# Kernel optimization log

Measured on AMD Instinct MI355X. Metric: run time of the kernel, lower is better.

## Reference

```python
import jax, jax.numpy as jnp
import numpy as np

N_NODES = 50000
N_EDGES = 800000
D = 128
LN_EPS = 1e-5


def setup_inputs() -> dict:
    key = jax.random.key(0)
    ks = jax.random.split(key, 8)
    s = 1.0 / np.sqrt(D)
    return {
        "x": jax.random.normal(ks[0], (N_NODES, D), jnp.float32),
        "edge_index": jax.random.randint(ks[1], (2, N_EDGES), 0, N_NODES, jnp.int64),
        "W1l": jax.random.normal(ks[2], (D, D), jnp.float32) * s,
        "b1l": jnp.zeros((D,), jnp.float32),
        "W1r": jax.random.normal(ks[3], (D, D), jnp.float32) * s,
        "W2l": jax.random.normal(ks[4], (D, D), jnp.float32) * s,
        "b2l": jnp.zeros((D,), jnp.float32),
        "W2r": jax.random.normal(ks[5], (D, D), jnp.float32) * s,
        "ln_w": jnp.ones((D,), jnp.float32),
        "ln_b": jnp.zeros((D,), jnp.float32),
    }


def _sage_conv(h, edge_index, Wl, bl, Wr):
    # PyG SAGEConv (mean aggr): out = lin_l(mean_{j in N(i)} h_j) + lin_r(h_i)
    src, dst = edge_index[0], edge_index[1]
    n = h.shape[0]
    msg_sum = jax.ops.segment_sum(h[src], dst, num_segments=n)      # [N, D]
    cnt = jax.ops.segment_sum(jnp.ones_like(src, h.dtype), dst, num_segments=n)
    mean = msg_sum / jnp.maximum(cnt, 1.0)[:, None]                  # 0 for isolated
    return mean @ Wl.T + bl + h @ Wr.T


def _layer_norm(h, w, b):
    mu = jnp.mean(h, axis=-1, keepdims=True)
    var = jnp.mean(jnp.square(h - mu), axis=-1, keepdims=True)
    return (h - mu) * jax.lax.rsqrt(var + LN_EPS) * w + b


def reference(x, edge_index, W1l, b1l, W1r, W2l, b2l, W2r, ln_w, ln_b):
    h = jax.nn.relu(_sage_conv(x, edge_index, W1l, b1l, W1r))
    h = jax.nn.relu(_sage_conv(h, edge_index, W2l, b2l, W2r))
    return _layer_norm(h, ln_w, ln_b)
```

## Files before the change

### kernel.cpp

```cpp
#include <hip/hip_runtime.h>

#define DN 128
#define LS 136

typedef short s16x8 __attribute__((ext_vector_type(8)));
typedef float f32x4 __attribute__((ext_vector_type(4)));

__device__ __forceinline__ float bf2f(unsigned short u) {
    union { unsigned int i; float f; } v; v.i = ((unsigned int)u) << 16; return v.f;
}
__device__ __forceinline__ unsigned short f2bf(float f) {
    union { float f; unsigned int i; } v; v.f = f;
    unsigned int r = v.i + 0x7fffu + ((v.i >> 16) & 1u);
    return (unsigned short)(r >> 16);
}
__device__ __forceinline__ float lo16(unsigned int u) { return bf2f((unsigned short)(u & 0xffffu)); }
__device__ __forceinline__ float hi16(unsigned int u) { return bf2f((unsigned short)(u >> 16)); }
__device__ __forceinline__ unsigned int pack2(float x, float y) {
    return (unsigned int)f2bf(x) | ((unsigned int)f2bf(y) << 16);
}
__device__ __forceinline__ float ldx(const void* p, size_t i, int f32) {
    return f32 ? ((const float*)p)[i] : bf2f(((const unsigned short*)p)[i]);
}

__global__ void k_diag(unsigned short* out, int cnt, float val) {
    unsigned short v = f2bf(val);
    for (int i = blockIdx.x * blockDim.x + threadIdx.x; i < cnt; i += gridDim.x * blockDim.x)
        out[i] = v;
}

__global__ void k_probe(const void* x, const void* w, const int* e, int* flags) {
    int g = blockIdx.x * 256 + threadIdx.x;
    const unsigned short* xu = (const unsigned short*)x;
    int hitx = 0, hitw = 0, hite = 0;
    for (int i = g; i < 65536; i += 32768)
        if ((xu[i] & 0x7F80u) == 0x7F80u) hitx = 1;
    const unsigned short* wu = (const unsigned short*)w;
    if (g < 16384 && (wu[g] & 0x7F80u) == 0x7F80u) hitw = 1;
    if (g < 1000 && e[2 * g + 1] != 0) hite = 1;
    if (hitx) atomicOr(&flags[0], 1);
    if (hitw) atomicOr(&flags[2], 1);
    if (hite) atomicOr(&flags[1], 1);
}


__global__ __launch_bounds__(1024) void k_packhist(
        const int* e, const void* x,
        const void* W1l, const void* W1r, const void* W2l, const void* W2r,
        const void* b1l, const void* b2l, const void* lnw, const void* lnb,
        const int* flags, unsigned int* packed, int* cnt,
        unsigned int* h1, unsigned int* wb, float* biasf, float* lnf,
        int E, int n, int cc) {
    __shared__ int hist[256];
    const int t = threadIdx.x, b = blockIdx.x;
    const int nthr = gridDim.x * 1024;
    const int g = b * 1024 + t;
    if (t < 256) hist[t] = 0;
    __syncthreads();
    const int is64 = (flags[1] == 0);
    const int xf = flags[0];
    const int wf = flags[2];
    const int b0 = b * 4096;
#pragma unroll
    for (int k = 0; k < 4; ++k) {
        int i = b0 + t + k * 1024;
        if (i < E) {
            int d = is64 ? e[2 * (E + i)] : e[E + i];
            int s = is64 ? e[2 * i] : e[i];
            if ((unsigned)s >= (unsigned)n) s = 0;
            unsigned int key = ((unsigned)d < (unsigned)n)
                             ? (((unsigned)d << 16) | (unsigned)s) : 0xFFFF0000u;
            packed[i] = key;
            atomicAdd(&hist[key >> 24], 1);
        }
    }
    if (xf) {
        const float* xp = (const float*)x;
        for (int i = g; i < cc; i += nthr) {
            float2 f = *(const float2*)(xp + 2 * (size_t)i);
            h1[i] = pack2(f.x, f.y);
        }
    } else {
        const unsigned int* xp = (const unsigned int*)x;
        for (int i = g; i < cc; i += nthr) h1[i] = xp[i];
    }
    for (int i = g; i < 32768; i += nthr) {
        int m = i >> 13, el = i & 8191;
        const void* W = (m == 0) ? W1l : (m == 1) ? W1r : (m == 2) ? W2l : W2r;
        unsigned int v;
        if (wf) {
            float2 f = *(const float2*)((const float*)W + 2 * (size_t)el);
            v = pack2(f.x, f.y);
        } else {
            v = ((const unsigned int*)W)[el];
        }
        wb[(size_t)m * 8192 + el] = v;
    }
    if (g < 512) {
        float v;
        if (g < 128)      v = ldx(b1l, g, wf);
        else if (g < 256) v = ldx(b2l, g - 128, wf);
        else if (g < 384) v = ldx(lnw, g - 256, wf);
        else              v = ldx(lnb, g - 384, wf);
        if (g < 256) biasf[g] = v; else lnf[g - 256] = v;
    }
    __syncthreads();
    if (t < 256 && hist[t]) atomicAdd(&cnt[t], hist[t]);
}

__device__ __forceinline__ void scan_cnt(const int* cnt, int* sbase, int t) {
    if (t < 64) {
        int c0 = cnt[4 * t], c1 = cnt[4 * t + 1], c2 = cnt[4 * t + 2], c3 = cnt[4 * t + 3];
        int tot = c0 + c1 + c2 + c3, pre = tot;
#pragma unroll
        for (int off = 1; off < 64; off <<= 1) {
            int u = __shfl_up(pre, off, 64);
            if (t >= off) pre += u;
        }
        int e0 = pre - tot;
        sbase[4 * t] = e0; sbase[4 * t + 1] = e0 + c0;
        sbase[4 * t + 2] = e0 + c0 + c1; sbase[4 * t + 3] = e0 + c0 + c1 + c2;
        if (t == 63) sbase[256] = pre;
    }
}

__global__ __launch_bounds__(1024) void k_p1scat(const unsigned int* in, const int* cnt,
                                                 int* rsv, unsigned int* out, int E) {
    __shared__ int hist[256], lcur[256], gbase[256], sbase[257];
    int t = threadIdx.x;
    int b0 = blockIdx.x * 4096;
    int nb = E - b0; if (nb > 4096) nb = 4096;
    if (t < 256) hist[t] = 0;
    __syncthreads();
    unsigned int v[4];
#pragma unroll
    for (int k = 0; k < 4; ++k) {
        int i = t + k * 1024;
        v[k] = (i < nb) ? in[b0 + i] : 0u;
        if (i < nb) atomicAdd(&hist[v[k] >> 24], 1);
    }
    scan_cnt(cnt, sbase, t);
    __syncthreads();
    if (t < 256) {
        lcur[t] = 0;
        if (hist[t]) gbase[t] = sbase[t] + atomicAdd(&rsv[t], hist[t]);
    }
    __syncthreads();
#pragma unroll
    for (int k = 0; k < 4; ++k) {
        int i = t + k * 1024;
        if (i < nb) {
            unsigned int d = v[k] >> 24;
            int p = atomicAdd(&lcur[d], 1);
            out[gbase[d] + p] = v[k];
        }
    }
}

__global__ __launch_bounds__(1024) void k_p2(const unsigned int* in, const int* cnt,
                                             int* rowp, int* col, int n) {
    __shared__ int hist[256], cur[256], sbase[257];
    int t = threadIdx.x;
    int b = blockIdx.x;
    if (t < 256) hist[t] = 0;
    scan_cnt(cnt, sbase, t);
    __syncthreads();
    int lo = sbase[b], hi = sbase[b + 1];
    if (b == 0 && t == 0) rowp[n] = sbase[196];
    for (int i = lo + t; i < hi; i += 1024)
        atomicAdd(&hist[(in[i] >> 16) & 0xFFu], 1);
    __syncthreads();
    if (t < 64) {
        int h0 = hist[4 * t], h1 = hist[4 * t + 1], h2 = hist[4 * t + 2], h3 = hist[4 * t + 3];
        int tot = h0 + h1 + h2 + h3;
        int pre = tot;
#pragma unroll
        for (int off = 1; off < 64; off <<= 1) {
            int u = __shfl_up(pre, off, 64);
            if (t >= off) pre += u;
        }
        int e0 = pre - tot;
        int e1 = e0 + h0, e2 = e1 + h1, e3 = e2 + h2;
        cur[4 * t] = e0; cur[4 * t + 1] = e1; cur[4 * t + 2] = e2; cur[4 * t + 3] = e3;
        int d0 = b * 256 + 4 * t;
        if (d0 < n)     rowp[d0]     = lo + e0;
        if (d0 + 1 < n) rowp[d0 + 1] = lo + e1;
        if (d0 + 2 < n) rowp[d0 + 2] = lo + e2;
        if (d0 + 3 < n) rowp[d0 + 3] = lo + e3;
    }
    __syncthreads();
    for (int i = lo + t; i < hi; i += 1024) {
        unsigned int v = in[i];
        int p = atomicAdd(&cur[(v >> 16) & 0xFFu], 1);
        col[lo + p] = (int)(v & 0xFFFFu);
    }
}

__global__ void k_gather(const int* rowp, const int* col, const unsigned int* hp,
                         unsigned int* M, int n) {
    int row = blockIdx.x * 4 + (threadIdx.x >> 6);
    if (row >= n) return;
    const int L = threadIdx.x & 63;
    int b = rowp[row], e = rowp[row + 1];
    float s0 = 0.f, s1 = 0.f;
    for (int base = b; base < e; base += 64) {
        int cnt = e - base; if (cnt > 64) cnt = 64;
        int myc = (L < cnt) ? col[base + L] : 0;
        int j = 0;
        for (; j + 8 <= cnt; j += 8) {
            int a0 = __shfl(myc, j + 0, 64);
            int a1 = __shfl(myc, j + 1, 64);
            int a2 = __shfl(myc, j + 2, 64);
            int a3 = __shfl(myc, j + 3, 64);
            int a4 = __shfl(myc, j + 4, 64);
            int a5 = __shfl(myc, j + 5, 64);
            int a6 = __shfl(myc, j + 6, 64);
            int a7 = __shfl(myc, j + 7, 64);
            unsigned int u0 = hp[(size_t)a0 * 64 + L];
            unsigned int u1 = hp[(size_t)a1 * 64 + L];
            unsigned int u2 = hp[(size_t)a2 * 64 + L];
            unsigned int u3 = hp[(size_t)a3 * 64 + L];
            unsigned int u4 = hp[(size_t)a4 * 64 + L];
            unsigned int u5 = hp[(size_t)a5 * 64 + L];
            unsigned int u6 = hp[(size_t)a6 * 64 + L];
            unsigned int u7 = hp[(size_t)a7 * 64 + L];
            s0 += lo16(u0); s1 += hi16(u0);
            s0 += lo16(u1); s1 += hi16(u1);
            s0 += lo16(u2); s1 += hi16(u2);
            s0 += lo16(u3); s1 += hi16(u3);
            s0 += lo16(u4); s1 += hi16(u4);
            s0 += lo16(u5); s1 += hi16(u5);
            s0 += lo16(u6); s1 += hi16(u6);
            s0 += lo16(u7); s1 += hi16(u7);
        }
        for (; j + 4 <= cnt; j += 4) {
            int a0 = __shfl(myc, j + 0, 64);
            int a1 = __shfl(myc, j + 1, 64);
            int a2 = __shfl(myc, j + 2, 64);
            int a3 = __shfl(myc, j + 3, 64);
            unsigned int u0 = hp[(size_t)a0 * 64 + L];
            unsigned int u1 = hp[(size_t)a1 * 64 + L];
            unsigned int u2 = hp[(size_t)a2 * 64 + L];
            unsigned int u3 = hp[(size_t)a3 * 64 + L];
            s0 += lo16(u0); s1 += hi16(u0);
            s0 += lo16(u1); s1 += hi16(u1);
            s0 += lo16(u2); s1 += hi16(u2);
            s0 += lo16(u3); s1 += hi16(u3);
        }
        for (; j < cnt; ++j) {
            int s = __shfl(myc, j, 64);
            unsigned int u = hp[(size_t)s * 64 + L];
            s0 += lo16(u); s1 += hi16(u);
        }
    }
    int d = e - b; if (d < 1) d = 1;
    float inv = 1.0f / (float)d;
    M[(size_t)row * 64 + L] = pack2(s0 * inv, s1 * inv);
}

__global__ __launch_bounds__(256) void k_gemm(
        const unsigned int* M, const unsigned int* hin,
        const unsigned int* wbl, const unsigned int* wbr,
        const float* biasf, const int* flags,
        void* hout, int n, int do_ln, const float* lnwf, const float* lnbf) {
    __shared__ unsigned short sA[64 * LS];
    __shared__ unsigned short sB[128 * LS];
    unsigned int* sAu = (unsigned int*)sA;
    unsigned int* sBu = (unsigned int*)sB;
    const int t = threadIdx.x;
    const int i0 = blockIdx.x * 64;
    const int lane = t & 63, wv = t >> 6, ln15 = lane & 15, quad = lane >> 4;

    f32x4 acc[8];
#pragma unroll
    for (int i = 0; i < 8; ++i) { f32x4 z = {0.f, 0.f, 0.f, 0.f}; acc[i] = z; }

    for (int phase = 0; phase < 2; ++phase) {
        const unsigned int* A = phase ? hin : M;
#pragma unroll
        for (int i = 0; i < 4; ++i) {
            int idx = t + i * 256, r = idx >> 4, c4 = (idx & 15) * 4;
            int node = i0 + r;
            uint4 v = make_uint4(0u, 0u, 0u, 0u);
            if (node < n) v = *(const uint4*)(A + (size_t)node * 64 + c4);
            *(uint4*)(sAu + r * 68 + c4) = v;
        }
        const unsigned int* W = phase ? wbr : wbl;
#pragma unroll
        for (int i = 0; i < 8; ++i) {
            int idx = t + i * 256, r = idx >> 4, c4 = (idx & 15) * 4;
            *(uint4*)(sBu + r * 68 + c4) = *(const uint4*)(W + (size_t)r * 64 + c4);
        }
        __syncthreads();

        const int mrow = wv * 16;
#pragma unroll
        for (int ks = 0; ks < 4; ++ks) {
            s16x8 a = *(const s16x8*)&sA[(mrow + ln15) * LS + ks * 32 + quad * 8];
#pragma unroll
            for (int nt = 0; nt < 8; ++nt) {
                s16x8 bfr = *(const s16x8*)&sB[(nt * 16 + ln15) * LS + ks * 32 + quad * 8];
                acc[nt] = __builtin_amdgcn_mfma_f32_16x16x32_bf16(a, bfr, acc[nt], 0, 0, 0);
            }
        }
        __syncthreads();
    }

#pragma unroll
    for (int nt = 0; nt < 8; ++nt) {
        float bs = biasf[nt * 16 + ln15];
#pragma unroll
        for (int r = 0; r < 4; ++r) {
            float v = acc[nt][r] + bs;
            acc[nt][r] = (v > 0.f) ? v : 0.f;
        }
    }

    if (!do_ln) {
#pragma unroll
        for (int nt = 0; nt < 8; ++nt) {
            int colv = nt * 16 + ln15;
#pragma unroll
            for (int r = 0; r < 4; ++r) {
                int node = i0 + wv * 16 + quad * 4 + r;
                if (node < n)
                    ((unsigned short*)hout)[(size_t)node * DN + colv] = f2bf(acc[nt][r]);
            }
        }
        return;
    }

    const int mix = (flags[0] != flags[2]);
    if (mix) {
#pragma unroll
        for (int nt = 0; nt < 8; ++nt) {
            int colv = nt * 16 + ln15;
#pragma unroll
            for (int r = 0; r < 4; ++r) {
                int node = i0 + wv * 16 + quad * 4 + r;
                if (node < n)
                    ((unsigned short*)hout)[(size_t)node * DN + colv] = 0x442F;
            }
        }
        return;
    }
    const int outf32 = (flags[0] && flags[2]);
    float lw[8], lb[8];
#pragma unroll
    for (int nt = 0; nt < 8; ++nt) {
        lw[nt] = lnwf[nt * 16 + ln15];
        lb[nt] = lnbf[nt * 16 + ln15];
    }
#pragma unroll
    for (int r = 0; r < 4; ++r) {
        float s = 0.f;
#pragma unroll
        for (int nt = 0; nt < 8; ++nt) s += acc[nt][r];
#pragma unroll
        for (int off = 1; off < 16; off <<= 1) s += __shfl_xor(s, off, 64);
        float mu = s * (1.0f / 128.0f);
        float q = 0.f;
#pragma unroll
        for (int nt = 0; nt < 8; ++nt) { float d = acc[nt][r] - mu; q += d * d; }
#pragma unroll
        for (int off = 1; off < 16; off <<= 1) q += __shfl_xor(q, off, 64);
        float rs = rsqrtf(q * (1.0f / 128.0f) + 1e-5f);
        int node = i0 + wv * 16 + quad * 4 + r;
        if (node < n) {
#pragma unroll
            for (int nt = 0; nt < 8; ++nt) {
                int colv = nt * 16 + ln15;
                float o = (acc[nt][r] - mu) * rs * lw[nt] + lb[nt];
                if (outf32) ((float*)hout)[(size_t)node * DN + colv] = o;
                else ((unsigned short*)hout)[(size_t)node * DN + colv] = f2bf(o);
            }
        }
    }
}

extern "C" void kernel_launch(void* const* d_in, const int* in_sizes, int n_in,
                              void* d_out, int out_size, void* d_ws, size_t ws_size,
                              hipStream_t stream) {
    const int N_EXP = 50000, E_EXP = 800000;

    const size_t sz_flags  = 256;
    const size_t sz_rowp   = (((size_t)(N_EXP + 1) * 4) + 255) & ~(size_t)255;
    const size_t sz_cursor = (((size_t)N_EXP * 4) + 255) & ~(size_t)255;
    const size_t sz_col    = (((size_t)E_EXP * 4) + 255) & ~(size_t)255;
    const size_t sz_M      = (size_t)N_EXP * 64 * 4;
    const size_t sz_h      = (size_t)N_EXP * DN * 2;
    const size_t need = sz_flags + sz_rowp + sz_cursor + sz_col + sz_M + sz_h;

    float diag = 0.f;
    if (in_sizes[0] != N_EXP * DN) diag += 1000.f;
    if (in_sizes[1] != 2 * E_EXP)  diag += 2000.f;
    if (n_in != 10)                diag += 4000.f;
    if (out_size != N_EXP * DN)    diag += 8000.f;
    if (ws_size < need)            diag += 16000.f;
    if (diag != 0.f) {
        k_diag<<<1024, 256, 0, stream>>>((unsigned short*)d_out, N_EXP * DN, diag);
        return;
    }

    const void* x   = d_in[0];
    const int*  ei  = (const int*)d_in[1];
    const void* W1l = d_in[2];
    const void* b1l = d_in[3];
    const void* W1r = d_in[4];
    const void* W2l = d_in[5];
    const void* b2l = d_in[6];
    const void* W2r = d_in[7];
    const void* lnw = d_in[8];
    const void* lnb = d_in[9];

    const int n = N_EXP, E = E_EXP;
    int cc = n * 64;

    char* ws = (char*)d_ws;
    int* rowp   = (int*)(ws + sz_flags);
    int* small  = (int*)(ws + sz_flags + sz_rowp);
    int* col    = (int*)(ws + sz_flags + sz_rowp + sz_cursor);
    unsigned int* M  = (unsigned int*)(ws + sz_flags + sz_rowp + sz_cursor + sz_col);
    unsigned int* h1 = (unsigned int*)(ws + sz_flags + sz_rowp + sz_cursor + sz_col + sz_M);

    int* flags = small;
    int* cnt   = small + 64;
    int* rsv   = small + 320;
    unsigned int* wb    = (unsigned int*)(small + 576);
    float* biasf = (float*)(small + 33344);
    float* lnf   = (float*)(small + 33600);
    unsigned int* packed0 = (unsigned int*)col;
    unsigned int* packed1 = (unsigned int*)M;

    hipMemsetAsync(small, 0, 2304, stream);

    k_probe<<<128, 256, 0, stream>>>(x, W1l, ei, flags);

    int P1B = (E + 4095) / 4096;
    k_packhist<<<P1B, 1024, 0, stream>>>(ei, x, W1l, W1r, W2l, W2r,
                                         b1l, b2l, lnw, lnb, flags,
                                         packed0, cnt, h1, wb, biasf, lnf, E, n, cc);
    k_p1scat<<<P1B, 1024, 0, stream>>>(packed0, cnt, rsv, packed1, E);
    k_p2<<<P1B, 1024, 0, stream>>>(packed1, cnt, rowp, col, n);

    int gb = (n + 3) / 4;
    int mb = (n + 63) / 64;

    k_gather<<<gb, 256, 0, stream>>>(rowp, col, h1, M, n);
    k_gemm<<<mb, 256, 0, stream>>>(M, h1, wb, wb + 8192, biasf, flags,
                                   h1, n, 0, nullptr, nullptr);
    k_gather<<<gb, 256, 0, stream>>>(rowp, col, h1, M, n);
    k_gemm<<<mb, 256, 0, stream>>>(M, h1, wb + 16384, wb + 24576, biasf + 128, flags,
                                   d_out, n, 1, lnf, lnf + 128);
}
```

Baseline: 211.2 us.

## Fold input-format probe into packhist and double GEMM row tile

Removes the separate probe kernel and its flag memset. Each packhist block now rescans a prefix of x, W1l and the edge array into shared flags and writes them to global memory. The GEMM kernel moves from 64-row/256-thread tiles to 128-row/512-thread tiles, which halves how often the weight tile is reloaded per node and cuts the block count. The trade-off is redundant probe reads in every packhist block and higher LDS use per GEMM block.

```diff
diff --git a/kernel.cpp b/kernel.cpp
--- a/kernel.cpp
+++ b/kernel.cpp
@@ -29,37 +29,47 @@
         out[i] = v;
 }
 
-__global__ void k_probe(const void* x, const void* w, const int* e, int* flags) {
-    int g = blockIdx.x * 256 + threadIdx.x;
-    const unsigned short* xu = (const unsigned short*)x;
-    int hitx = 0, hitw = 0, hite = 0;
-    for (int i = g; i < 65536; i += 32768)
-        if ((xu[i] & 0x7F80u) == 0x7F80u) hitx = 1;
-    const unsigned short* wu = (const unsigned short*)w;
-    if (g < 16384 && (wu[g] & 0x7F80u) == 0x7F80u) hitw = 1;
-    if (g < 1000 && e[2 * g + 1] != 0) hite = 1;
-    if (hitx) atomicOr(&flags[0], 1);
-    if (hitw) atomicOr(&flags[2], 1);
-    if (hite) atomicOr(&flags[1], 1);
-}
-
 
 __global__ __launch_bounds__(1024) void k_packhist(
         const int* e, const void* x,
         const void* W1l, const void* W1r, const void* W2l, const void* W2r,
         const void* b1l, const void* b2l, const void* lnw, const void* lnb,
-        const int* flags, unsigned int* packed, int* cnt,
+        int* flags, unsigned int* packed, int* cnt,
         unsigned int* h1, unsigned int* wb, float* biasf, float* lnf,
         int E, int n, int cc) {
     __shared__ int hist[256];
+    __shared__ int s_fl[3];
     const int t = threadIdx.x, b = blockIdx.x;
     const int nthr = gridDim.x * 1024;
     const int g = b * 1024 + t;
+
+    if (t < 3) s_fl[t] = 0;
     if (t < 256) hist[t] = 0;
     __syncthreads();
-    const int is64 = (flags[1] == 0);
-    const int xf = flags[0];
-    const int wf = flags[2];
+    {
+        const unsigned int* xu = (const unsigned int*)x;
+        int hit = 0;
+#pragma unroll
+        for (int i = t; i < 32768; i += 1024) {
+            unsigned int u = xu[i];
+            if (((u & 0x7F80u) == 0x7F80u) || (((u >> 16) & 0x7F80u) == 0x7F80u)) hit = 1;
+        }
+        if (hit) atomicOr(&s_fl[0], 1);
+        const unsigned int* wu = (const unsigned int*)W1l;
+        hit = 0;
+#pragma unroll
+        for (int i = t; i < 8192; i += 1024) {
+            unsigned int u = wu[i];
+            if (((u & 0x7F80u) == 0x7F80u) || (((u >> 16) & 0x7F80u) == 0x7F80u)) hit = 1;
+        }
+        if (hit) atomicOr(&s_fl[2], 1);
+        if (t < 1000 && e[2 * t + 1] != 0) atomicOr(&s_fl[1], 1);
+    }
+    __syncthreads();
+    const int xf = s_fl[0], is64 = (s_fl[1] == 0), wf = s_fl[2];
+    if (t < 3 && b == 0) { }
+    if (t == 0) { flags[0] = s_fl[0]; flags[1] = s_fl[1]; flags[2] = s_fl[2]; }
+
     const int b0 = b * 4096;
 #pragma unroll
     for (int k = 0; k < 4; ++k) {
@@ -258,17 +268,17 @@
     M[(size_t)row * 64 + L] = pack2(s0 * inv, s1 * inv);
 }
 
-__global__ __launch_bounds__(256) void k_gemm(
+__global__ __launch_bounds__(512) void k_gemm(
         const unsigned int* M, const unsigned int* hin,
         const unsigned int* wbl, const unsigned int* wbr,
         const float* biasf, const int* flags,
         void* hout, int n, int do_ln, const float* lnwf, const float* lnbf) {
-    __shared__ unsigned short sA[64 * LS];
+    __shared__ unsigned short sA[128 * LS];
     __shared__ unsigned short sB[128 * LS];
     unsigned int* sAu = (unsigned int*)sA;
     unsigned int* sBu = (unsigned int*)sB;
     const int t = threadIdx.x;
-    const int i0 = blockIdx.x * 64;
+    const int i0 = blockIdx.x * 128;
     const int lane = t & 63, wv = t >> 6, ln15 = lane & 15, quad = lane >> 4;
 
     f32x4 acc[8];
@@ -279,7 +289,7 @@
         const unsigned int* A = phase ? hin : M;
 #pragma unroll
         for (int i = 0; i < 4; ++i) {
-            int idx = t + i * 256, r = idx >> 4, c4 = (idx & 15) * 4;
+            int idx = t + i * 512, r = idx >> 4, c4 = (idx & 15) * 4;
             int node = i0 + r;
             uint4 v = make_uint4(0u, 0u, 0u, 0u);
             if (node < n) v = *(const uint4*)(A + (size_t)node * 64 + c4);
@@ -287,8 +297,8 @@
         }
         const unsigned int* W = phase ? wbr : wbl;
 #pragma unroll
-        for (int i = 0; i < 8; ++i) {
-            int idx = t + i * 256, r = idx >> 4, c4 = (idx & 15) * 4;
+        for (int i = 0; i < 4; ++i) {
+            int idx = t + i * 512, r = idx >> 4, c4 = (idx & 15) * 4;
             *(uint4*)(sBu + r * 68 + c4) = *(const uint4*)(W + (size_t)r * 64 + c4);
         }
         __syncthreads();
@@ -432,9 +442,7 @@
     unsigned int* packed0 = (unsigned int*)col;
     unsigned int* packed1 = (unsigned int*)M;
 
-    hipMemsetAsync(small, 0, 2304, stream);
-
-    k_probe<<<128, 256, 0, stream>>>(x, W1l, ei, flags);
+    hipMemsetAsync(cnt, 0, 2048, stream);
 
     int P1B = (E + 4095) / 4096;
     k_packhist<<<P1B, 1024, 0, stream>>>(ei, x, W1l, W1r, W2l, W2r,
@@ -444,12 +452,12 @@
     k_p2<<<P1B, 1024, 0, stream>>>(packed1, cnt, rowp, col, n);
 
     int gb = (n + 3) / 4;
-    int mb = (n + 63) / 64;
+    int mb = (n + 127) / 128;
 
     k_gather<<<gb, 256, 0, stream>>>(rowp, col, h1, M, n);
-    k_gemm<<<mb, 256, 0, stream>>>(M, h1, wb, wb + 8192, biasf, flags,
+    k_gemm<<<mb, 512, 0, stream>>>(M, h1, wb, wb + 8192, biasf, flags,
                                    h1, n, 0, nullptr, nullptr);
     k_gather<<<gb, 256, 0, stream>>>(rowp, col, h1, M, n);
-    k_gemm<<<mb, 256, 0, stream>>>(M, h1, wb + 16384, wb + 24576, biasf + 128, flags,
+    k_gemm<<<mb, 512, 0, stream>>>(M, h1, wb + 16384, wb + 24576, biasf + 128, flags,
                                    d_out, n, 1, lnf, lnf + 128);
 }
```

New measurement: 211.1 us. About the same (-0.1%).
